# Optimization experiments

Measured on AMD Instinct MI355X. Metric: run time of the kernel, lower is better.

Reference implementation:

```python
import jax, jax.numpy as jnp
import numpy as np

jax.config.update("jax_enable_x64", True)  # exact int64 fixed-point requantization

QMIN, QMAX = 0, 255  # 8-bit asymmetric activations


def _mul_m0_shift(acc, M0, shift):
    """gemmlowp-style fixed-point rescale: round((acc*M0)>>31) >> shift (rounding)."""
    prod = acc.astype(jnp.int64) * M0.astype(jnp.int64)
    nudge = jnp.where(prod >= 0, jnp.int64(1 << 30), jnp.int64(1 - (1 << 30)))
    hi = (prod + nudge) >> 31  # rounding-doubling high mul
    sh = shift.astype(jnp.int64)
    return (hi + (jnp.int64(1) << (sh - 1))) >> sh  # rounding right shift


def _requant(acc, M0, shift, z_out):
    return jnp.clip(_mul_m0_shift(acc, M0, shift) + z_out, QMIN, QMAX).astype(jnp.int32)


def _qconv(q, w, z_in, M0, shift, z_out, pad):
    # int8-style conv: subtract input zero-point, integer accumulate (exact in fp32
    # since |acc| < 2^24 by construction), then fixed-point requantize.
    xf = (q - z_in).astype(jnp.float32)
    acc = jax.lax.conv_general_dilated(
        xf, w, (1, 1), [(pad, pad), (pad, pad)],
        dimension_numbers=("NCHW", "OIHW", "NCHW"))
    return _requant(jnp.round(acc).astype(jnp.int64), M0, shift, z_out)


def _qbn(q, z_in, w, b, M0, shift, z_out):
    # fused quantized BN: per-channel integer affine + fixed-point requantize
    acc = (q.astype(jnp.int64) - z_in) * w.astype(jnp.int64)[None, :, None, None] \
          + b.astype(jnp.int64)[None, :, None, None]
    return _requant(acc, M0, shift, z_out)


def setup_inputs() -> dict:
    key = jax.random.key(0)
    ks = jax.random.split(key, 10)
    B, Cin, H, W = 32, 256, 56, 56
    width, Cout = 64, 256
    x = jax.random.randint(ks[0], (B, Cin, H, W), 0, 256, dtype=jnp.int32)
    w1 = jax.random.randint(ks[1], (width, Cin, 1, 1), -63, 64).astype(jnp.float32)
    w2 = jax.random.randint(ks[2], (width, width, 3, 3), -63, 64).astype(jnp.float32)
    w3 = jax.random.randint(ks[3], (Cout, width, 1, 1), -63, 64).astype(jnp.float32)
    bn1_w = jax.random.randint(ks[4], (width,), 100, 160).astype(jnp.float32)
    bn1_b = jax.random.randint(ks[5], (width,), -1000, 1000).astype(jnp.float32)
    bn2_w = jax.random.randint(ks[6], (width,), 100, 160).astype(jnp.float32)
    bn2_b = jax.random.randint(ks[7], (width,), -1000, 1000).astype(jnp.float32)
    bn3_w = jax.random.randint(ks[8], (Cout,), 100, 160).astype(jnp.float32)
    bn3_b = jax.random.randint(ks[9], (Cout,), -1000, 1000).astype(jnp.float32)
    conv_zin = jnp.array([128, 128, 128], jnp.int32)
    conv_m0 = jnp.array([1518500250] * 3, jnp.int32)
    conv_shift = jnp.array([9, 9, 9], jnp.int32)
    conv_zout = jnp.array([128, 128, 128], jnp.int32)
    bn_m0 = jnp.array([1073741824] * 3, jnp.int32)
    bn_shift = jnp.array([6, 6, 6], jnp.int32)
    bn_zout = jnp.array([128, 128, 128], jnp.int32)
    add_z = jnp.array([128, 128], jnp.int32)
    add_m0 = jnp.array([1073741824] * 2, jnp.int32)
    add_shift = jnp.array([1, 1], jnp.int32)
    add_zout = jnp.array(128, jnp.int32)
    return dict(x=x, w1=w1, w2=w2, w3=w3,
                bn1_w=bn1_w, bn1_b=bn1_b, bn2_w=bn2_w, bn2_b=bn2_b,
                bn3_w=bn3_w, bn3_b=bn3_b,
                conv_zin=conv_zin, conv_m0=conv_m0, conv_shift=conv_shift,
                conv_zout=conv_zout, bn_m0=bn_m0, bn_shift=bn_shift,
                bn_zout=bn_zout, add_z=add_z, add_m0=add_m0,
                add_shift=add_shift, add_zout=add_zout)


def reference(x, w1, w2, w3, bn1_w, bn1_b, bn2_w, bn2_b, bn3_w, bn3_b,
              conv_zin, conv_m0, conv_shift, conv_zout,
              bn_m0, bn_shift, bn_zout,
              add_z, add_m0, add_shift, add_zout):
    identity = x  # a_bit == target_bit -> rescale_matrix path skipped, conv_x = x
    out = _qconv(x, w1, conv_zin[0], conv_m0[0], conv_shift[0], conv_zout[0], 0)
    out = _qbn(out, conv_zout[0], bn1_w, bn1_b, bn_m0[0], bn_shift[0], bn_zout[0])
    out = _qconv(out, w2, conv_zin[1], conv_m0[1], conv_shift[1], conv_zout[1], 1)
    out = _qbn(out, conv_zout[1], bn2_w, bn2_b, bn_m0[1], bn_shift[1], bn_zout[1])
    out = _qconv(out, w3, conv_zin[2], conv_m0[2], conv_shift[2], conv_zout[2], 0)
    out = _qbn(out, conv_zout[2], bn3_w, bn3_b, bn_m0[2], bn_shift[2], bn_zout[2])
    # QuantizedAdd: rescale both branches to the output scale, add, clamp
    ra = _mul_m0_shift(identity.astype(jnp.int64) - add_z[0], add_m0[0], add_shift[0])
    rb = _mul_m0_shift(out.astype(jnp.int64) - add_z[1], add_m0[1], add_shift[1])
    return jnp.clip(ra + rb + add_zout, QMIN, QMAX).astype(jnp.int32)
```

## Files before the change

kernel.cpp:

```cpp
#include <hip/hip_runtime.h>


typedef int v4i __attribute__((ext_vector_type(4)));

#define BATCH 32
#define CIN 256
#define CMID 64
#define HW 3136
#define W56 56

#define WP_BYTES ((size_t)68 * 64 * 16)
#define WSUM_BYTES ((size_t)64 * 4)

__device__ __forceinline__ int rq_apply(int acc, int m0, long long cp, long long cn,
                                        int shm1, int zo) {
    long long prod = (long long)acc * m0;
    prod += (prod >= 0) ? cp : cn;
    int hi = (int)((unsigned long long)prod >> 32);
    int v = (hi >> shm1) + zo;
    return v < 0 ? 0 : (v > 255 ? 255 : v);
}

__device__ __forceinline__ int ms_apply(int xin, int m0, long long cp, long long cn,
                                        int shm1) {
    long long prod = (long long)xin * m0;
    prod += (prod >= 0) ? cp : cn;
    return ((int)((unsigned long long)prod >> 32)) >> shm1;
}

__device__ __forceinline__ unsigned int pk4x(int a0, int a1, int a2, int a3) {
    unsigned p01 = __builtin_amdgcn_perm((unsigned)a1, (unsigned)a0, 0x00000400u);
    unsigned p23 = __builtin_amdgcn_perm((unsigned)a3, (unsigned)a2, 0x04000000u);
    return __builtin_amdgcn_perm(p23, p01, 0x07060100u);
}

__device__ __forceinline__ void gll16(const int* g, void* l) {
    __builtin_amdgcn_global_load_lds(
        (const __attribute__((address_space(1))) unsigned int*)g,
        (__attribute__((address_space(3))) unsigned int*)l, 16, 0, 0);
}

__device__ __forceinline__ v4i pack16f(const float* src, int stride) {
    v4i r;
#pragma unroll
    for (int d = 0; d < 4; ++d) {
        unsigned int u = 0;
#pragma unroll
        for (int by = 0; by < 4; ++by) {
            int v = (int)src[(d * 4 + by) * stride];
            u |= ((unsigned int)(v & 255)) << (8 * by);
        }
        r[d] = (int)u;
    }
    return r;
}

__global__ __launch_bounds__(256) void k_prep(
    const float* __restrict__ w1, const float* __restrict__ w2,
    const float* __restrict__ w3, v4i* __restrict__ wp, int* __restrict__ wsum)
{
    if (blockIdx.x < 17) {
        int id = blockIdx.x * 256 + threadIdx.x;
        int fid = id >> 6, lane = id & 63;
        int col = lane & 15, ci0 = (lane >> 4) * 16;
        const float* src;
        int stride;
        if (fid < 16) {
            int wv = fid >> 2, ks = fid & 3;
            src = w1 + (size_t)(wv * 16 + col) * 256 + ks * 64 + ci0;
            stride = 1;
        } else if (fid < 52) {
            int i = fid - 16, wv = i / 9, t = i - wv * 9;
            src = w2 + ((size_t)(wv * 16 + col) * 64 + ci0) * 9 + t;
            stride = 9;
        } else {
            int s = fid - 52;
            src = w3 + (size_t)(s * 16 + col) * 64 + ci0;
            stride = 1;
        }
        wp[fid * 64 + lane] = pack16f(src, stride);
    } else {
        int ch = threadIdx.x >> 2, t4 = threadIdx.x & 3;
        int s = 0;
        for (int i = 0; i < 64; ++i) s += (int)w1[(size_t)ch * 256 + t4 * 64 + i];
        s += __shfl_xor(s, 1);
        s += __shfl_xor(s, 2);
        if (t4 == 0) wsum[ch] = s;
    }
}

__global__ __launch_bounds__(256, 4) void k_conv1(
    const int* __restrict__ x, const v4i* __restrict__ wp1,
    const int* __restrict__ wsum1,
    const float* __restrict__ bn_w, const float* __restrict__ bn_b,
    const int* __restrict__ conv_zin, const int* __restrict__ conv_m0,
    const int* __restrict__ conv_shift, const int* __restrict__ conv_zout,
    const int* __restrict__ bn_m0, const int* __restrict__ bn_shift,
    const int* __restrict__ bn_zout, signed char* __restrict__ t1)
{
    __shared__ v4i sm[560];
    const int tid = threadIdx.x, lane = tid & 63, wv = tid >> 6;
    const int col = lane & 15, koff = lane >> 4;
    const int b = blockIdx.y;
    const int hw0 = blockIdx.x * 112;
    const int co0 = wv * 16;

    v4i a[4];
#pragma unroll
    for (int ks = 0; ks < 4; ++ks) a[ks] = wp1[(wv * 4 + ks) * 64 + lane];

    const int cg = tid & 7, q = tid >> 3;
    const bool act = q < 28;
    const int* xbase = x + (size_t)b * CIN * HW + hw0 + 4 * q;

    v4i xa[8], xa2[8];
    if (act) {
#pragma unroll
        for (int j = 0; j < 8; ++j)
            xa[j] = *(const v4i*)(xbase + (size_t)(cg * 8 + j) * HW);
    }

    v4i acc[7];
#pragma unroll
    for (int i = 0; i < 7; ++i) acc[i] = (v4i){0, 0, 0, 0};

    unsigned long long* smu = (unsigned long long*)sm;
#pragma unroll
    for (int ks = 0; ks < 4; ++ks) {
        if (ks) __syncthreads();
        if (act) {
#pragma unroll
            for (int p = 0; p < 4; ++p) {
                unsigned lo = pk4x(xa[0][p], xa[1][p], xa[2][p], xa[3][p]) ^ 0x80808080u;
                unsigned hi = pk4x(xa[4][p], xa[5][p], xa[6][p], xa[7][p]) ^ 0x80808080u;
                smu[(q * 4 + p) * 10 + cg] = ((unsigned long long)hi << 32) | lo;
            }
        }
        __syncthreads();
        if (ks < 3 && act) {
#pragma unroll
            for (int j = 0; j < 8; ++j)
                xa2[j] = *(const v4i*)(xbase + (size_t)((ks + 1) * 64 + cg * 8 + j) * HW);
        }
#pragma unroll
        for (int nt = 0; nt < 7; ++nt) {
            v4i bf = sm[(nt * 16 + col) * 5 + koff];
            acc[nt] = __builtin_amdgcn_mfma_i32_16x16x64_i8(a[ks], bf, acc[nt], 0, 0, 0);
        }
        if (ks < 3) {
#pragma unroll
            for (int j = 0; j < 8; ++j) xa[j] = xa2[j];
        }
    }

    const int zin = conv_zin[0];
    const int corr0 = 128 - zin;
    const int cm0 = conv_m0[0], csh = conv_shift[0], czo = conv_zout[0];
    const int bm0 = bn_m0[0], bsh = bn_shift[0], bzo = bn_zout[0];
    const int zin2 = conv_zin[1];
    const long long cbv = 1LL << (30 + csh);
    const long long ccp = cbv + (1LL << 30), ccn = cbv + 1 - (1LL << 30);
    const int cshm1 = csh - 1;
    const long long bbv = 1LL << (30 + bsh);
    const long long bcp = bbv + (1LL << 30), bcn = bbv + 1 - (1LL << 30);
    const int bshm1 = bsh - 1;
    const int rowb = koff * 4;
    int bw[4], bbx[4], ws[4];
#pragma unroll
    for (int r = 0; r < 4; ++r) {
        bw[r] = (int)bn_w[co0 + rowb + r];
        bbx[r] = (int)bn_b[co0 + rowb + r] - czo * bw[r];
        ws[r] = wsum1[co0 + rowb + r];
    }
#pragma unroll
    for (int nt = 0; nt < 7; ++nt) {
        int n = b * HW + hw0 + nt * 16 + col;
        int e[4];
#pragma unroll
        for (int r = 0; r < 4; ++r) {
            int av = acc[nt][r] + corr0 * ws[r];
            int qv = rq_apply(av, cm0, ccp, ccn, cshm1, czo);
            int a2 = qv * bw[r] + bbx[r];
            int q2 = rq_apply(a2, bm0, bcp, bcn, bshm1, bzo);
            e[r] = q2 - zin2;
        }
        *(unsigned*)(t1 + (size_t)n * 64 + co0 + rowb) = pk4x(e[0], e[1], e[2], e[3]);
    }
}

__global__ __launch_bounds__(256, 3) void k_conv23(
    const signed char* __restrict__ t1, const v4i* __restrict__ wp2,
    const v4i* __restrict__ wp3,
    const float* __restrict__ bn2_w, const float* __restrict__ bn2_b,
    const float* __restrict__ bn3_w, const float* __restrict__ bn3_b,
    const int* __restrict__ x,
    const int* __restrict__ conv_zin, const int* __restrict__ conv_m0,
    const int* __restrict__ conv_shift, const int* __restrict__ conv_zout,
    const int* __restrict__ bn_m0, const int* __restrict__ bn_shift,
    const int* __restrict__ bn_zout,
    const int* __restrict__ add_z, const int* __restrict__ add_m0,
    const int* __restrict__ add_shift, const int* __restrict__ add_zout,
    int* __restrict__ out)
{
    __shared__ v4i sm[840];
    __shared__ v4i t2s[320];
    __shared__ int xs[2][64][64];
    const int tid = threadIdx.x, lane = tid & 63, wv = tid >> 6;
    const int col = lane & 15, koff = lane >> 4;
    const int b = blockIdx.y;
    const int r0 = blockIdx.x;
    const int co0 = wv * 16, rowb = koff * 4;

    v4i a[9];
#pragma unroll
    for (int t = 0; t < 9; ++t) a[t] = wp2[(wv * 9 + t) * 64 + lane];
    v4i a3x[4];
#pragma unroll
    for (int s = 0; s < 4; ++s) a3x[s] = wp3[(wv * 4 + s) * 64 + lane];

    const v4i* t1v = (const v4i*)t1;
#pragma unroll
    for (int k = 0; k < 3; ++k) {
        int idx = tid + k * 256;
        if (idx < 672) {
            int pixl = idx >> 2, part = idx & 3;
            int lrow = pixl / W56, gw = pixl - lrow * W56;
            int grow = r0 - 1 + lrow;
            v4i v = (v4i){0, 0, 0, 0};
            if ((unsigned)grow < 56u)
                v = t1v[((size_t)b * HW + grow * W56 + gw) * 4 + part];
            sm[pixl * 5 + part] = v;
        }
    }
    __syncthreads();

    const int* gsrc = x + (size_t)b * CIN * HW + (size_t)r0 * W56;
    int pxl = (lane & 15) * 4;
    if (pxl > 52) pxl = 52;
    const int chsub = lane >> 4;
    auto stage = [&](int t) {
        const int chb = wv * 64 + t * 16 + chsub;
#pragma unroll
        for (int j = 0; j < 4; ++j)
            gll16(gsrc + (size_t)(chb + j * 4) * HW + pxl,
                  &xs[t & 1][wv * 16 + j * 4][0]);
    };
    stage(0);
    stage(1);

    v4i acc[4];
#pragma unroll
    for (int i = 0; i < 4; ++i) acc[i] = (v4i){0, 0, 0, 0};

#pragma unroll
    for (int kh = 0; kh < 3; ++kh) {
#pragma unroll
        for (int kw = 0; kw < 3; ++kw) {
            v4i af = a[kh * 3 + kw];
#pragma unroll
            for (int nt = 0; nt < 4; ++nt) {
                int sw = nt * 16 + col + kw - 1;
                bool valid = (unsigned)sw < 56u;
                v4i bf = sm[(kh * W56 + (valid ? sw : 0)) * 5 + koff];
                if (!valid) { bf[0] = 0; bf[1] = 0; bf[2] = 0; bf[3] = 0; }
                acc[nt] = __builtin_amdgcn_mfma_i32_16x16x64_i8(af, bf, acc[nt], 0, 0, 0);
            }
        }
    }

    {
        const int cm0 = conv_m0[1], csh = conv_shift[1], czo = conv_zout[1];
        const int bm0 = bn_m0[1], bsh = bn_shift[1], bzo = bn_zout[1];
        const int zin3 = conv_zin[2];
        const long long cbv = 1LL << (30 + csh);
        const long long ccp = cbv + (1LL << 30), ccn = cbv + 1 - (1LL << 30);
        const int cshm1 = csh - 1;
        const long long bbv = 1LL << (30 + bsh);
        const long long bcp = bbv + (1LL << 30), bcn = bbv + 1 - (1LL << 30);
        const int bshm1 = bsh - 1;
        int bw[4], bbx[4];
#pragma unroll
        for (int r = 0; r < 4; ++r) {
            bw[r] = (int)bn2_w[co0 + rowb + r];
            bbx[r] = (int)bn2_b[co0 + rowb + r] - czo * bw[r];
        }
#pragma unroll
        for (int nt = 0; nt < 4; ++nt) {
            int pix = nt * 16 + col;
            int e[4];
#pragma unroll
            for (int r = 0; r < 4; ++r) {
                int qv = rq_apply(acc[nt][r], cm0, ccp, ccn, cshm1, czo);
                int a2 = qv * bw[r] + bbx[r];
                int q2 = rq_apply(a2, bm0, bcp, bcn, bshm1, bzo);
                e[r] = q2 - zin3;
            }
            *(unsigned*)((char*)t2s + (size_t)(pix * 5 + wv) * 16 + koff * 4) =
                pk4x(e[0], e[1], e[2], e[3]);
        }
    }

    const int cm0 = conv_m0[2], csh = conv_shift[2], czo = conv_zout[2];
    const int bm0 = bn_m0[2], bsh = bn_shift[2], bzo = bn_zout[2];
    const long long cb3 = 1LL << (30 + csh);
    const long long ccp = cb3 + (1LL << 30), ccn = cb3 + 1 - (1LL << 30);
    const int cshm1 = csh - 1;
    const long long bb3 = 1LL << (30 + bsh);
    const long long bcp = bb3 + (1LL << 30), bcn = bb3 + 1 - (1LL << 30);
    const int bshm1 = bsh - 1;
    const int az0 = add_z[0], az1 = add_z[1];
    const int am0 = add_m0[0], am1 = add_m0[1];
    const int ash0 = add_shift[0], ash1 = add_shift[1];
    const long long a0b = 1LL << (30 + ash0);
    const long long acp0 = a0b + (1LL << 30), acn0 = a0b + 1 - (1LL << 30);
    const int ashm0 = ash0 - 1;
    const long long a1b = 1LL << (30 + ash1);
    const long long acp1 = a1b + (1LL << 30), acn1 = a1b + 1 - (1LL << 30);
    const int ashm1 = ash1 - 1;
    const int azout = add_zout[0];
    int bw3[4][4], bbx3[4][4];
#pragma unroll
    for (int s = 0; s < 4; ++s)
#pragma unroll
        for (int r = 0; r < 4; ++r) {
            bw3[s][r] = (int)bn3_w[wv * 64 + s * 16 + rowb + r];
            bbx3[s][r] = (int)bn3_b[wv * 64 + s * 16 + rowb + r] - czo * bw3[s][r];
        }

    __syncthreads();

    int* ob = out + (size_t)b * CIN * HW + (size_t)r0 * W56;

#pragma unroll
    for (int t = 0; t < 4; ++t) {
        const int c0 = wv * 64 + t * 16;
        v4i acc3[4];
#pragma unroll
        for (int i = 0; i < 4; ++i) acc3[i] = (v4i){0, 0, 0, 0};
#pragma unroll
        for (int nt = 0; nt < 4; ++nt) {
            v4i bf = t2s[(nt * 16 + col) * 5 + koff];
            acc3[nt] = __builtin_amdgcn_mfma_i32_16x16x64_i8(a3x[t], bf, acc3[nt], 0, 0, 0);
        }
        asm volatile("s_waitcnt vmcnt(4)" ::: "memory");
        __builtin_amdgcn_sched_barrier(0);
#pragma unroll
        for (int nt = 0; nt < 4; ++nt) {
            int px = nt * 16 + col;
            bool st = px < 56;
#pragma unroll
            for (int r = 0; r < 4; ++r) {
                int xr = xs[t & 1][co0 + rowb + r][px];
                int qv = rq_apply(acc3[nt][r], cm0, ccp, ccn, cshm1, czo);
                int a2 = qv * bw3[t][r] + bbx3[t][r];
                int q2 = rq_apply(a2, bm0, bcp, bcn, bshm1, bzo);
                int ra = ms_apply(xr - az0, am0, acp0, acn0, ashm0);
                int rb = ms_apply(q2 - az1, am1, acp1, acn1, ashm1);
                int res = ra + rb + azout;
                res = res < 0 ? 0 : (res > 255 ? 255 : res);
                if (st) ob[(size_t)(c0 + rowb + r) * HW + px] = res;
            }
        }
        if (t < 2) {
            asm volatile("s_waitcnt lgkmcnt(0)" ::: "memory");
            __builtin_amdgcn_sched_barrier(0);
            stage(t + 2);
        }
    }
}

extern "C" void kernel_launch(void* const* d_in, const int* in_sizes, int n_in,
                              void* d_out, int out_size, void* d_ws, size_t ws_size,
                              hipStream_t stream) {
    const int* x = (const int*)d_in[0];
    const float* w1 = (const float*)d_in[1];
    const float* w2 = (const float*)d_in[2];
    const float* w3 = (const float*)d_in[3];
    const float* bn1_w = (const float*)d_in[4];
    const float* bn1_b = (const float*)d_in[5];
    const float* bn2_w = (const float*)d_in[6];
    const float* bn2_b = (const float*)d_in[7];
    const float* bn3_w = (const float*)d_in[8];
    const float* bn3_b = (const float*)d_in[9];
    const int* conv_zin = (const int*)d_in[10];
    const int* conv_m0 = (const int*)d_in[11];
    const int* conv_shift = (const int*)d_in[12];
    const int* conv_zout = (const int*)d_in[13];
    const int* bn_m0 = (const int*)d_in[14];
    const int* bn_shift = (const int*)d_in[15];
    const int* bn_zout = (const int*)d_in[16];
    const int* add_z = (const int*)d_in[17];
    const int* add_m0 = (const int*)d_in[18];
    const int* add_shift = (const int*)d_in[19];
    const int* add_zout = (const int*)d_in[20];

    v4i* wp = (v4i*)d_ws;
    int* wsum1 = (int*)((char*)d_ws + WP_BYTES);
    signed char* t1 = (signed char*)d_ws + WP_BYTES + WSUM_BYTES;

    const v4i* wp1 = wp;
    const v4i* wp2 = wp + 16 * 64;
    const v4i* wp3 = wp + 52 * 64;

    k_prep<<<dim3(18), dim3(256), 0, stream>>>(w1, w2, w3, wp, wsum1);
    k_conv1<<<dim3(28, 32), dim3(256), 0, stream>>>(x, wp1, wsum1, bn1_w, bn1_b,
        conv_zin, conv_m0, conv_shift, conv_zout, bn_m0, bn_shift, bn_zout, t1);
    k_conv23<<<dim3(56, 32), dim3(256), 0, stream>>>(t1, wp2, wp3,
        bn2_w, bn2_b, bn3_w, bn3_b, x,
        conv_zin, conv_m0, conv_shift, conv_zout, bn_m0, bn_shift, bn_zout,
        add_z, add_m0, add_shift, add_zout, (int*)d_out);
}
```

Baseline: 287.6 us.

## Write packed int8 copy of x in conv1 and read it for residual

Conv1 already packs x into signed bytes for its MFMA tiles, and now it also writes that packed copy (NHWC, 256 bytes per pixel) to workspace. Conv23 reads the residual from this compact int8 buffer instead of re-reading the int32 NCHW input through an LDS double buffer. This cuts the second full read of x from 4 bytes to 1 byte per element and frees 32KB of LDS, so launch bounds go from 3 to 4 blocks. The cost is an extra global write in conv1 and strided per-pixel byte loads in conv23.

```diff
diff --git a/kernel.cpp b/kernel.cpp
--- a/kernel.cpp
+++ b/kernel.cpp
@@ -11,6 +11,7 @@
 
 #define WP_BYTES ((size_t)68 * 64 * 16)
 #define WSUM_BYTES ((size_t)64 * 4)
+#define T1_BYTES ((size_t)BATCH * HW * CMID)
 
 __device__ __forceinline__ int rq_apply(int acc, int m0, long long cp, long long cn,
                                         int shm1, int zo) {
@@ -32,12 +33,6 @@
     unsigned p01 = __builtin_amdgcn_perm((unsigned)a1, (unsigned)a0, 0x00000400u);
     unsigned p23 = __builtin_amdgcn_perm((unsigned)a3, (unsigned)a2, 0x04000000u);
     return __builtin_amdgcn_perm(p23, p01, 0x07060100u);
-}
-
-__device__ __forceinline__ void gll16(const int* g, void* l) {
-    __builtin_amdgcn_global_load_lds(
-        (const __attribute__((address_space(1))) unsigned int*)g,
-        (__attribute__((address_space(3))) unsigned int*)l, 16, 0, 0);
 }
 
 __device__ __forceinline__ v4i pack16f(const float* src, int stride) {
@@ -96,7 +91,8 @@
     const int* __restrict__ conv_zin, const int* __restrict__ conv_m0,
     const int* __restrict__ conv_shift, const int* __restrict__ conv_zout,
     const int* __restrict__ bn_m0, const int* __restrict__ bn_shift,
-    const int* __restrict__ bn_zout, signed char* __restrict__ t1)
+    const int* __restrict__ bn_zout, signed char* __restrict__ t1,
+    unsigned char* __restrict__ xq)
 {
     __shared__ v4i sm[560];
     const int tid = threadIdx.x, lane = tid & 63, wv = tid >> 6;
@@ -112,6 +108,7 @@
     const int cg = tid & 7, q = tid >> 3;
     const bool act = q < 28;
     const int* xbase = x + (size_t)b * CIN * HW + hw0 + 4 * q;
+    unsigned char* xqb = xq + ((size_t)b * HW + hw0 + 4 * q) * 256 + cg * 8;
 
     v4i xa[8], xa2[8];
     if (act) {
@@ -133,7 +130,9 @@
             for (int p = 0; p < 4; ++p) {
                 unsigned lo = pk4x(xa[0][p], xa[1][p], xa[2][p], xa[3][p]) ^ 0x80808080u;
                 unsigned hi = pk4x(xa[4][p], xa[5][p], xa[6][p], xa[7][p]) ^ 0x80808080u;
-                smu[(q * 4 + p) * 10 + cg] = ((unsigned long long)hi << 32) | lo;
+                unsigned long long pv = ((unsigned long long)hi << 32) | lo;
+                smu[(q * 4 + p) * 10 + cg] = pv;
+                *(unsigned long long*)(xqb + (size_t)p * 256 + ks * 64) = pv;
             }
         }
         __syncthreads();
@@ -188,12 +187,12 @@
     }
 }
 
-__global__ __launch_bounds__(256, 3) void k_conv23(
+__global__ __launch_bounds__(256, 4) void k_conv23(
     const signed char* __restrict__ t1, const v4i* __restrict__ wp2,
     const v4i* __restrict__ wp3,
     const float* __restrict__ bn2_w, const float* __restrict__ bn2_b,
     const float* __restrict__ bn3_w, const float* __restrict__ bn3_b,
-    const int* __restrict__ x,
+    const unsigned char* __restrict__ xq,
     const int* __restrict__ conv_zin, const int* __restrict__ conv_m0,
     const int* __restrict__ conv_shift, const int* __restrict__ conv_zout,
     const int* __restrict__ bn_m0, const int* __restrict__ bn_shift,
@@ -204,7 +203,6 @@
 {
     __shared__ v4i sm[840];
     __shared__ v4i t2s[320];
-    __shared__ int xs[2][64][64];
     const int tid = threadIdx.x, lane = tid & 63, wv = tid >> 6;
     const int col = lane & 15, koff = lane >> 4;
     const int b = blockIdx.y;
@@ -234,20 +232,6 @@
     }
     __syncthreads();
 
-    const int* gsrc = x + (size_t)b * CIN * HW + (size_t)r0 * W56;
-    int pxl = (lane & 15) * 4;
-    if (pxl > 52) pxl = 52;
-    const int chsub = lane >> 4;
-    auto stage = [&](int t) {
-        const int chb = wv * 64 + t * 16 + chsub;
-#pragma unroll
-        for (int j = 0; j < 4; ++j)
-            gll16(gsrc + (size_t)(chb + j * 4) * HW + pxl,
-                  &xs[t & 1][wv * 16 + j * 4][0]);
-    };
-    stage(0);
-    stage(1);
-
     v4i acc[4];
 #pragma unroll
     for (int i = 0; i < 4; ++i) acc[i] = (v4i){0, 0, 0, 0};
@@ -267,6 +251,20 @@
             }
         }
     }
+
+    int pxc[4];
+#pragma unroll
+    for (int nt = 0; nt < 4; ++nt) {
+        int px = nt * 16 + col;
+        pxc[nt] = px < 56 ? px : 55;
+    }
+    const unsigned char* xqb = xq + ((size_t)b * HW + r0 * W56) * 256 + wv * 64 + rowb;
+    int xqv[4][4];
+#pragma unroll
+    for (int t = 0; t < 4; ++t)
+#pragma unroll
+        for (int nt = 0; nt < 4; ++nt)
+            xqv[t][nt] = *(const int*)(xqb + (size_t)pxc[nt] * 256 + t * 16);
 
     {
         const int cm0 = conv_m0[1], csh = conv_shift[1], czo = conv_zout[1];
@@ -299,6 +297,7 @@
                 pk4x(e[0], e[1], e[2], e[3]);
         }
     }
+    __syncthreads();
 
     const int cm0 = conv_m0[2], csh = conv_shift[2], czo = conv_zout[2];
     const int bm0 = bn_m0[2], bsh = bn_shift[2], bzo = bn_zout[2];
@@ -309,6 +308,7 @@
     const long long bcp = bb3 + (1LL << 30), bcn = bb3 + 1 - (1LL << 30);
     const int bshm1 = bsh - 1;
     const int az0 = add_z[0], az1 = add_z[1];
+    const int corr = 128 - az0;
     const int am0 = add_m0[0], am1 = add_m0[1];
     const int ash0 = add_shift[0], ash1 = add_shift[1];
     const long long a0b = 1LL << (30 + ash0);
@@ -318,6 +318,7 @@
     const long long acp1 = a1b + (1LL << 30), acn1 = a1b + 1 - (1LL << 30);
     const int ashm1 = ash1 - 1;
     const int azout = add_zout[0];
+
     int bw3[4][4], bbx3[4][4];
 #pragma unroll
     for (int s = 0; s < 4; ++s)
@@ -327,7 +328,9 @@
             bbx3[s][r] = (int)bn3_b[wv * 64 + s * 16 + rowb + r] - czo * bw3[s][r];
         }
 
-    __syncthreads();
+    v4i bf[4];
+#pragma unroll
+    for (int nt = 0; nt < 4; ++nt) bf[nt] = t2s[(nt * 16 + col) * 5 + koff];
 
     int* ob = out + (size_t)b * CIN * HW + (size_t)r0 * W56;
 
@@ -338,33 +341,24 @@
 #pragma unroll
         for (int i = 0; i < 4; ++i) acc3[i] = (v4i){0, 0, 0, 0};
 #pragma unroll
-        for (int nt = 0; nt < 4; ++nt) {
-            v4i bf = t2s[(nt * 16 + col) * 5 + koff];
-            acc3[nt] = __builtin_amdgcn_mfma_i32_16x16x64_i8(a3x[t], bf, acc3[nt], 0, 0, 0);
-        }
-        asm volatile("s_waitcnt vmcnt(4)" ::: "memory");
-        __builtin_amdgcn_sched_barrier(0);
+        for (int nt = 0; nt < 4; ++nt)
+            acc3[nt] = __builtin_amdgcn_mfma_i32_16x16x64_i8(a3x[t], bf[nt], acc3[nt], 0, 0, 0);
 #pragma unroll
         for (int nt = 0; nt < 4; ++nt) {
             int px = nt * 16 + col;
             bool st = px < 56;
 #pragma unroll
             for (int r = 0; r < 4; ++r) {
-                int xr = xs[t & 1][co0 + rowb + r][px];
+                int sx = (int)(signed char)(((unsigned)xqv[t][nt]) >> (8 * r));
                 int qv = rq_apply(acc3[nt][r], cm0, ccp, ccn, cshm1, czo);
                 int a2 = qv * bw3[t][r] + bbx3[t][r];
                 int q2 = rq_apply(a2, bm0, bcp, bcn, bshm1, bzo);
-                int ra = ms_apply(xr - az0, am0, acp0, acn0, ashm0);
+                int ra = ms_apply(sx + corr, am0, acp0, acn0, ashm0);
                 int rb = ms_apply(q2 - az1, am1, acp1, acn1, ashm1);
                 int res = ra + rb + azout;
                 res = res < 0 ? 0 : (res > 255 ? 255 : res);
                 if (st) ob[(size_t)(c0 + rowb + r) * HW + px] = res;
             }
-        }
-        if (t < 2) {
-            asm volatile("s_waitcnt lgkmcnt(0)" ::: "memory");
-            __builtin_amdgcn_sched_barrier(0);
-            stage(t + 2);
         }
     }
 }
@@ -397,6 +391,7 @@
     v4i* wp = (v4i*)d_ws;
     int* wsum1 = (int*)((char*)d_ws + WP_BYTES);
     signed char* t1 = (signed char*)d_ws + WP_BYTES + WSUM_BYTES;
+    unsigned char* xq = (unsigned char*)t1 + T1_BYTES;
 
     const v4i* wp1 = wp;
     const v4i* wp2 = wp + 16 * 64;
@@ -404,9 +399,9 @@
 
     k_prep<<<dim3(18), dim3(256), 0, stream>>>(w1, w2, w3, wp, wsum1);
     k_conv1<<<dim3(28, 32), dim3(256), 0, stream>>>(x, wp1, wsum1, bn1_w, bn1_b,
-        conv_zin, conv_m0, conv_shift, conv_zout, bn_m0, bn_shift, bn_zout, t1);
+        conv_zin, conv_m0, conv_shift, conv_zout, bn_m0, bn_shift, bn_zout, t1, xq);
     k_conv23<<<dim3(56, 32), dim3(256), 0, stream>>>(t1, wp2, wp3,
-        bn2_w, bn2_b, bn3_w, bn3_b, x,
+        bn2_w, bn2_b, bn3_w, bn3_b, xq,
         conv_zin, conv_m0, conv_shift, conv_zout, bn_m0, bn_shift, bn_zout,
         add_z, add_m0, add_shift, add_zout, (int*)d_out);
 }
```

Result: no change. 291.4 us (+1.3%).
